# Optimization experiments

Measured on AMD Instinct MI355X. Metric: run time of the kernel, lower is better.

Reference implementation:

```python
import jax, jax.numpy as jnp
import numpy as np

SIGMA = 1e-4
GAMMA = 1e-4
ZNEAR = 1.0
ZFAR = 100.0
EPS = 1e-10
BG = (1.0, 1.0, 1.0)

N, H, W, K = 4, 512, 512, 8
V, F = 100000, 200000


def setup_inputs() -> dict:
    key = jax.random.key(0)
    k1, k2, k3, k4, k5, k6 = jax.random.split(key, 6)
    pix_to_face = jax.random.randint(k1, (N, H, W, K), -1, F)  # -1 = background
    bary = jax.random.uniform(k2, (N, H, W, K, 3), dtype=jnp.float32)
    bary = bary / jnp.sum(bary, axis=-1, keepdims=True)  # valid barycentric
    zbuf = ZNEAR + (ZFAR - ZNEAR) * jax.random.uniform(k3, (N, H, W, K), dtype=jnp.float32)
    dists = 1e-4 * jax.random.normal(k4, (N, H, W, K), dtype=jnp.float32)
    verts_normals = jax.random.normal(k5, (V, 3), dtype=jnp.float32)
    verts_normals = verts_normals / jnp.linalg.norm(verts_normals, axis=-1, keepdims=True)
    faces = jax.random.randint(k6, (F, 3), 0, V)
    return {"pix_to_face": pix_to_face, "bary_coords": bary, "zbuf": zbuf,
            "dists": dists, "verts_normals": verts_normals, "faces": faces}


def reference(pix_to_face, bary_coords, zbuf, dists, verts_normals, faces):
    # --- NormalCalcuate: gather per-face vertex normals + barycentric interp ---
    faces_normals = verts_normals[faces]                      # (F, 3verts, 3)
    mask = pix_to_face >= 0                                    # (N,H,W,K)
    idx = jnp.maximum(pix_to_face, 0)
    attrs = faces_normals[idx]                                 # (N,H,W,K,3verts,3)
    pixel_normals = jnp.einsum('nhwkv,nhwkvd->nhwkd', bary_coords, attrs)
    pixel_normals = jnp.where(mask[..., None], pixel_normals, 0.0)

    # --- softmax_rgb_blend ---
    m = mask.astype(pixel_normals.dtype)
    prob_map = jax.nn.sigmoid(-dists / SIGMA) * m              # (N,H,W,K)
    z_inv = (ZFAR - zbuf) / (ZFAR - ZNEAR) * m                 # (N,H,W,K)
    z_inv_max = jnp.maximum(jnp.max(z_inv, axis=-1, keepdims=True), EPS)
    weights_num = prob_map * jnp.exp((z_inv - z_inv_max) / GAMMA)
    delta = jnp.maximum(jnp.exp((EPS - z_inv_max[..., 0]) / GAMMA), EPS)  # (N,H,W)
    denom = jnp.sum(weights_num, axis=-1) + delta              # (N,H,W)
    weighted_colors = jnp.einsum('nhwk,nhwkd->nhwd', weights_num, pixel_normals)
    bg = jnp.asarray(BG, dtype=pixel_normals.dtype)
    rgb = (weighted_colors + delta[..., None] * bg) / denom[..., None]  # (N,H,W,3)

    # --- F.normalize(dim=3) then (x+1)/2 ---
    norm = jnp.maximum(jnp.linalg.norm(rgb, axis=-1, keepdims=True), 1e-12)
    images = (rgb / norm + 1.0) / 2.0
    return images
```

## Files before the change

### kernel.cpp

```cpp
#include <hip/hip_runtime.h>

#define SIGMA_INV 1.0e4f
#define GAMMA_INV 1.0e4f
#define ZNEAR 1.0f
#define ZFAR 100.0f
#define EPSV 1e-10f

constexpr int KF = 8;
constexpr int NPIX = 4 * 512 * 512;
constexpr int NFACES = 200000;

__global__ __launch_bounds__(256) void pack_face_normals14(
    const int*   __restrict__ faces,
    const float* __restrict__ vnorm,
    uint4*       __restrict__ fn,
    int F)
{
    const int f = blockIdx.x * blockDim.x + threadIdx.x;
    if (f >= F) return;
    const int v[3] = { faces[f * 3 + 0], faces[f * 3 + 1], faces[f * 3 + 2] };

    unsigned long long lo = 0ull, hi = 0ull;
    int i = 0;
#pragma unroll
    for (int t = 0; t < 3; ++t) {
#pragma unroll
        for (int c = 0; c < 3; ++c, ++i) {
            const float x = vnorm[(size_t)v[t] * 3 + c];
            const unsigned long long code = (unsigned long long)(unsigned)
                __float2int_rn(fminf(fmaxf(x, -1.0f), 1.0f) * 8191.5f + 8191.5f);
            const int bp = 14 * i;
            if (bp < 64) {
                lo |= code << bp;
                if (bp > 50) hi |= code >> (64 - bp);
            } else {
                hi |= code << (bp - 64);
            }
        }
    }
    uint4 q;
    q.x = (unsigned)(lo & 0xFFFFFFFFull);
    q.y = (unsigned)(lo >> 32);
    q.z = (unsigned)(hi & 0xFFFFFFFFull);
    q.w = (unsigned)(hi >> 32);
    fn[f] = q;
}

__device__ __forceinline__ float dec14(const unsigned* w, int i) {
    const int bp = 14 * i;
    const int j = bp >> 5;
    const int off = bp & 31;
    unsigned long long u = (unsigned long long)w[j];
    if (j < 3) u |= (unsigned long long)w[j + 1] << 32;
    const unsigned code = (unsigned)(u >> off) & 0x3FFFu;
    return fmaf((float)code, 2.0f / 16383.0f, -1.0f);
}

__global__ __launch_bounds__(256) void normal_shader_q14(
    const int*   __restrict__ p2f,
    const float* __restrict__ bary,
    const float* __restrict__ zbuf,
    const float* __restrict__ dists,
    const uint4* __restrict__ fn,
    float*       __restrict__ out)
{
    const int p = blockIdx.x * blockDim.x + threadIdx.x;
    if (p >= NPIX) return;

    const int4* pf4 = reinterpret_cast<const int4*>(p2f + (size_t)p * KF);
    int4 fa = pf4[0], fb = pf4[1];
    int f[KF] = {fa.x, fa.y, fa.z, fa.w, fb.x, fb.y, fb.z, fb.w};

    uint4 q[KF];
#pragma unroll
    for (int k = 0; k < KF; ++k) {
        const int idx = f[k] < 0 ? 0 : f[k];
        q[k] = fn[idx];
    }

    const float4* z4 = reinterpret_cast<const float4*>(zbuf + (size_t)p * KF);
    float4 za = z4[0], zb = z4[1];
    float zv[KF] = {za.x, za.y, za.z, za.w, zb.x, zb.y, zb.z, zb.w};

    const float4* d4 = reinterpret_cast<const float4*>(dists + (size_t)p * KF);
    float4 da = d4[0], db = d4[1];
    float dv[KF] = {da.x, da.y, da.z, da.w, db.x, db.y, db.z, db.w};

    const float4* b4 = reinterpret_cast<const float4*>(bary + (size_t)p * KF * 3);
    float bc[KF * 3];
#pragma unroll
    for (int i = 0; i < 6; ++i) {
        float4 t = b4[i];
        bc[4 * i + 0] = t.x; bc[4 * i + 1] = t.y;
        bc[4 * i + 2] = t.z; bc[4 * i + 3] = t.w;
    }

    float zinv[KF], prob[KF];
    float zmax = EPSV;
#pragma unroll
    for (int k = 0; k < KF; ++k) {
        const bool m = f[k] >= 0;
        const float zi = m ? (ZFAR - zv[k]) * (1.0f / (ZFAR - ZNEAR)) : 0.0f;
        const float pr = m ? 1.0f / (1.0f + __expf(dv[k] * SIGMA_INV)) : 0.0f;
        zinv[k] = zi;
        prob[k] = pr;
        zmax = fmaxf(zmax, zi);
    }

    float accx = 0.0f, accy = 0.0f, accz = 0.0f, wtot = 0.0f;
#pragma unroll
    for (int k = 0; k < KF; ++k) {
        unsigned w[4] = { q[k].x, q[k].y, q[k].z, q[k].w };
        const float n0x = dec14(w, 0), n0y = dec14(w, 1), n0z = dec14(w, 2);
        const float n1x = dec14(w, 3), n1y = dec14(w, 4), n1z = dec14(w, 5);
        const float n2x = dec14(w, 6), n2y = dec14(w, 7), n2z = dec14(w, 8);
        const float b0 = bc[k * 3 + 0];
        const float b1 = bc[k * 3 + 1];
        const float b2 = bc[k * 3 + 2];
        const float nx = b0 * n0x + b1 * n1x + b2 * n2x;
        const float ny = b0 * n0y + b1 * n1y + b2 * n2y;
        const float nz = b0 * n0z + b1 * n1z + b2 * n2z;
        const float wgt = prob[k] * __expf((zinv[k] - zmax) * GAMMA_INV);
        wtot += wgt;
        accx = fmaf(wgt, nx, accx);
        accy = fmaf(wgt, ny, accy);
        accz = fmaf(wgt, nz, accz);
    }

    const float delta = fmaxf(__expf((EPSV - zmax) * GAMMA_INV), EPSV);
    const float inv_denom = 1.0f / (wtot + delta);
    const float r = (accx + delta) * inv_denom;
    const float g = (accy + delta) * inv_denom;
    const float b = (accz + delta) * inv_denom;

    const float nrm = sqrtf(r * r + g * g + b * b);
    const float invn = 1.0f / fmaxf(nrm, 1e-12f);

    float* o = out + (size_t)p * 3;
    o[0] = fmaf(r * invn, 0.5f, 0.5f);
    o[1] = fmaf(g * invn, 0.5f, 0.5f);
    o[2] = fmaf(b * invn, 0.5f, 0.5f);
}

__global__ __launch_bounds__(256) void normal_shader_direct(
    const int*   __restrict__ p2f,
    const float* __restrict__ bary,
    const float* __restrict__ zbuf,
    const float* __restrict__ dists,
    const float* __restrict__ vnorm,
    const int*   __restrict__ faces,
    float*       __restrict__ out)
{
    const int p = blockIdx.x * blockDim.x + threadIdx.x;
    if (p >= NPIX) return;

    const int4* pf4 = reinterpret_cast<const int4*>(p2f + (size_t)p * KF);
    int4 fa = pf4[0], fb = pf4[1];
    int f[KF] = {fa.x, fa.y, fa.z, fa.w, fb.x, fb.y, fb.z, fb.w};

    const float4* z4 = reinterpret_cast<const float4*>(zbuf + (size_t)p * KF);
    float4 za = z4[0], zb = z4[1];
    float zv[KF] = {za.x, za.y, za.z, za.w, zb.x, zb.y, zb.z, zb.w};

    const float4* d4 = reinterpret_cast<const float4*>(dists + (size_t)p * KF);
    float4 da = d4[0], db = d4[1];
    float dv[KF] = {da.x, da.y, da.z, da.w, db.x, db.y, db.z, db.w};

    const float4* b4 = reinterpret_cast<const float4*>(bary + (size_t)p * KF * 3);
    float bc[KF * 3];
#pragma unroll
    for (int i = 0; i < 6; ++i) {
        float4 t = b4[i];
        bc[4 * i + 0] = t.x; bc[4 * i + 1] = t.y;
        bc[4 * i + 2] = t.z; bc[4 * i + 3] = t.w;
    }

    float zinv[KF], prob[KF];
    float zmax = EPSV;
#pragma unroll
    for (int k = 0; k < KF; ++k) {
        const bool m = f[k] >= 0;
        const float zi = m ? (ZFAR - zv[k]) * (1.0f / (ZFAR - ZNEAR)) : 0.0f;
        const float pr = m ? 1.0f / (1.0f + __expf(dv[k] * SIGMA_INV)) : 0.0f;
        zinv[k] = zi;
        prob[k] = pr;
        zmax = fmaxf(zmax, zi);
    }

    float accx = 0.0f, accy = 0.0f, accz = 0.0f, wtot = 0.0f;
#pragma unroll
    for (int k = 0; k < KF; ++k) {
        const int idx = f[k] < 0 ? 0 : f[k];
        const int i3 = idx * 3;
        const int v0 = faces[i3 + 0];
        const int v1 = faces[i3 + 1];
        const int v2 = faces[i3 + 2];
        const float b0 = bc[k * 3 + 0];
        const float b1 = bc[k * 3 + 1];
        const float b2 = bc[k * 3 + 2];
        const float* n0 = vnorm + (size_t)v0 * 3;
        const float* n1 = vnorm + (size_t)v1 * 3;
        const float* n2 = vnorm + (size_t)v2 * 3;
        const float nx = b0 * n0[0] + b1 * n1[0] + b2 * n2[0];
        const float ny = b0 * n0[1] + b1 * n1[1] + b2 * n2[1];
        const float nz = b0 * n0[2] + b1 * n1[2] + b2 * n2[2];
        const float wgt = prob[k] * __expf((zinv[k] - zmax) * GAMMA_INV);
        wtot += wgt;
        accx = fmaf(wgt, nx, accx);
        accy = fmaf(wgt, ny, accy);
        accz = fmaf(wgt, nz, accz);
    }

    const float delta = fmaxf(__expf((EPSV - zmax) * GAMMA_INV), EPSV);
    const float inv_denom = 1.0f / (wtot + delta);
    const float r = (accx + delta) * inv_denom;
    const float g = (accy + delta) * inv_denom;
    const float b = (accz + delta) * inv_denom;

    const float nrm = sqrtf(r * r + g * g + b * b);
    const float invn = 1.0f / fmaxf(nrm, 1e-12f);

    float* o = out + (size_t)p * 3;
    o[0] = fmaf(r * invn, 0.5f, 0.5f);
    o[1] = fmaf(g * invn, 0.5f, 0.5f);
    o[2] = fmaf(b * invn, 0.5f, 0.5f);
}

extern "C" void kernel_launch(void* const* d_in, const int* in_sizes, int n_in,
                              void* d_out, int out_size, void* d_ws, size_t ws_size,
                              hipStream_t stream) {
    const int*   p2f   = (const int*)d_in[0];
    const float* bary  = (const float*)d_in[1];
    const float* zbuf  = (const float*)d_in[2];
    const float* dists = (const float*)d_in[3];
    const float* vnorm = (const float*)d_in[4];
    const int*   faces = (const int*)d_in[5];
    float* out = (float*)d_out;

    const int threads = 256;
    const size_t fn_bytes = (size_t)NFACES * sizeof(uint4);

    if (ws_size >= fn_bytes) {
        uint4* fn = (uint4*)d_ws;
        pack_face_normals14<<<(NFACES + threads - 1) / threads, threads, 0, stream>>>(
            faces, vnorm, fn, NFACES);
        normal_shader_q14<<<(NPIX + threads - 1) / threads, threads, 0, stream>>>(
            p2f, bary, zbuf, dists, fn, out);
    } else {
        normal_shader_direct<<<(NPIX + threads - 1) / threads, threads, 0, stream>>>(
            p2f, bary, zbuf, dists, vnorm, faces, out);
    }
}
```

Measured before the change: 258.8 us.

## Split each pixel across four lanes with shuffle reductions

The shading kernel now assigns four threads per pixel, each handling two of the eight faces, and combines zmax, weights and accumulated normals with wave shuffles. Each lane issues only two gathers and loads, so fewer registers are live and more memory requests can be in flight to hide gather latency. In exchange it launches four times as many threads, adds shuffle and instruction overhead, and switches from wide float4 loads to float2 loads.

```diff
diff --git a/kernel.cpp b/kernel.cpp
--- a/kernel.cpp
+++ b/kernel.cpp
@@ -56,7 +56,7 @@
     return fmaf((float)code, 2.0f / 16383.0f, -1.0f);
 }
 
-__global__ __launch_bounds__(256) void normal_shader_q14(
+__global__ __launch_bounds__(256) void normal_shader_q14_split(
     const int*   __restrict__ p2f,
     const float* __restrict__ bary,
     const float* __restrict__ zbuf,
@@ -64,82 +64,73 @@
     const uint4* __restrict__ fn,
     float*       __restrict__ out)
 {
-    const int p = blockIdx.x * blockDim.x + threadIdx.x;
+    const int t = blockIdx.x * blockDim.x + threadIdx.x;
+    const int p = t >> 2;
+    const int sub = t & 3;
     if (p >= NPIX) return;
 
-    const int4* pf4 = reinterpret_cast<const int4*>(p2f + (size_t)p * KF);
-    int4 fa = pf4[0], fb = pf4[1];
-    int f[KF] = {fa.x, fa.y, fa.z, fa.w, fb.x, fb.y, fb.z, fb.w};
-
-    uint4 q[KF];
-#pragma unroll
-    for (int k = 0; k < KF; ++k) {
-        const int idx = f[k] < 0 ? 0 : f[k];
-        q[k] = fn[idx];
-    }
-
-    const float4* z4 = reinterpret_cast<const float4*>(zbuf + (size_t)p * KF);
-    float4 za = z4[0], zb = z4[1];
-    float zv[KF] = {za.x, za.y, za.z, za.w, zb.x, zb.y, zb.z, zb.w};
-
-    const float4* d4 = reinterpret_cast<const float4*>(dists + (size_t)p * KF);
-    float4 da = d4[0], db = d4[1];
-    float dv[KF] = {da.x, da.y, da.z, da.w, db.x, db.y, db.z, db.w};
-
-    const float4* b4 = reinterpret_cast<const float4*>(bary + (size_t)p * KF * 3);
-    float bc[KF * 3];
-#pragma unroll
-    for (int i = 0; i < 6; ++i) {
-        float4 t = b4[i];
-        bc[4 * i + 0] = t.x; bc[4 * i + 1] = t.y;
-        bc[4 * i + 2] = t.z; bc[4 * i + 3] = t.w;
-    }
-
-    float zinv[KF], prob[KF];
-    float zmax = EPSV;
-#pragma unroll
-    for (int k = 0; k < KF; ++k) {
-        const bool m = f[k] >= 0;
-        const float zi = m ? (ZFAR - zv[k]) * (1.0f / (ZFAR - ZNEAR)) : 0.0f;
-        const float pr = m ? 1.0f / (1.0f + __expf(dv[k] * SIGMA_INV)) : 0.0f;
-        zinv[k] = zi;
-        prob[k] = pr;
-        zmax = fmaxf(zmax, zi);
-    }
-
-    float accx = 0.0f, accy = 0.0f, accz = 0.0f, wtot = 0.0f;
-#pragma unroll
-    for (int k = 0; k < KF; ++k) {
-        unsigned w[4] = { q[k].x, q[k].y, q[k].z, q[k].w };
-        const float n0x = dec14(w, 0), n0y = dec14(w, 1), n0z = dec14(w, 2);
-        const float n1x = dec14(w, 3), n1y = dec14(w, 4), n1z = dec14(w, 5);
-        const float n2x = dec14(w, 6), n2y = dec14(w, 7), n2z = dec14(w, 8);
-        const float b0 = bc[k * 3 + 0];
-        const float b1 = bc[k * 3 + 1];
-        const float b2 = bc[k * 3 + 2];
-        const float nx = b0 * n0x + b1 * n1x + b2 * n2x;
-        const float ny = b0 * n0y + b1 * n1y + b2 * n2y;
-        const float nz = b0 * n0z + b1 * n1z + b2 * n2z;
-        const float wgt = prob[k] * __expf((zinv[k] - zmax) * GAMMA_INV);
+    const int base = p * KF + sub * 2;
+
+    const int2   f2  = *reinterpret_cast<const int2*>(p2f + base);
+    const float2 z2  = *reinterpret_cast<const float2*>(zbuf + base);
+    const float2 d2  = *reinterpret_cast<const float2*>(dists + base);
+    const float2 b01 = *reinterpret_cast<const float2*>(bary + (size_t)base * 3 + 0);
+    const float2 b23 = *reinterpret_cast<const float2*>(bary + (size_t)base * 3 + 2);
+    const float2 b45 = *reinterpret_cast<const float2*>(bary + (size_t)base * 3 + 4);
+
+    const int i0 = f2.x < 0 ? 0 : f2.x;
+    const int i1 = f2.y < 0 ? 0 : f2.y;
+    const uint4 g0 = fn[i0];
+    const uint4 g1 = fn[i1];
+
+    const bool m0 = f2.x >= 0, m1 = f2.y >= 0;
+    const float zi0 = m0 ? (ZFAR - z2.x) * (1.0f / (ZFAR - ZNEAR)) : 0.0f;
+    const float zi1 = m1 ? (ZFAR - z2.y) * (1.0f / (ZFAR - ZNEAR)) : 0.0f;
+    const float pr0 = m0 ? 1.0f / (1.0f + __expf(d2.x * SIGMA_INV)) : 0.0f;
+    const float pr1 = m1 ? 1.0f / (1.0f + __expf(d2.y * SIGMA_INV)) : 0.0f;
+
+    float zmax = fmaxf(fmaxf(zi0, zi1), EPSV);
+    zmax = fmaxf(zmax, __shfl_xor(zmax, 1));
+    zmax = fmaxf(zmax, __shfl_xor(zmax, 2));
+
+    float ax, ay, az, wtot;
+    {
+        unsigned w[4] = { g0.x, g0.y, g0.z, g0.w };
+        const float nx = b01.x * dec14(w, 0) + b01.y * dec14(w, 3) + b23.x * dec14(w, 6);
+        const float ny = b01.x * dec14(w, 1) + b01.y * dec14(w, 4) + b23.x * dec14(w, 7);
+        const float nz = b01.x * dec14(w, 2) + b01.y * dec14(w, 5) + b23.x * dec14(w, 8);
+        const float wgt = pr0 * __expf((zi0 - zmax) * GAMMA_INV);
+        wtot = wgt;
+        ax = wgt * nx; ay = wgt * ny; az = wgt * nz;
+    }
+    {
+        unsigned w[4] = { g1.x, g1.y, g1.z, g1.w };
+        const float nx = b23.y * dec14(w, 0) + b45.x * dec14(w, 3) + b45.y * dec14(w, 6);
+        const float ny = b23.y * dec14(w, 1) + b45.x * dec14(w, 4) + b45.y * dec14(w, 7);
+        const float nz = b23.y * dec14(w, 2) + b45.x * dec14(w, 5) + b45.y * dec14(w, 8);
+        const float wgt = pr1 * __expf((zi1 - zmax) * GAMMA_INV);
         wtot += wgt;
-        accx = fmaf(wgt, nx, accx);
-        accy = fmaf(wgt, ny, accy);
-        accz = fmaf(wgt, nz, accz);
-    }
+        ax = fmaf(wgt, nx, ax); ay = fmaf(wgt, ny, ay); az = fmaf(wgt, nz, az);
+    }
+
+    wtot += __shfl_xor(wtot, 1);  wtot += __shfl_xor(wtot, 2);
+    ax   += __shfl_xor(ax, 1);    ax   += __shfl_xor(ax, 2);
+    ay   += __shfl_xor(ay, 1);    ay   += __shfl_xor(ay, 2);
+    az   += __shfl_xor(az, 1);    az   += __shfl_xor(az, 2);
 
     const float delta = fmaxf(__expf((EPSV - zmax) * GAMMA_INV), EPSV);
     const float inv_denom = 1.0f / (wtot + delta);
-    const float r = (accx + delta) * inv_denom;
-    const float g = (accy + delta) * inv_denom;
-    const float b = (accz + delta) * inv_denom;
+    const float r = (ax + delta) * inv_denom;
+    const float g = (ay + delta) * inv_denom;
+    const float b = (az + delta) * inv_denom;
 
     const float nrm = sqrtf(r * r + g * g + b * b);
     const float invn = 1.0f / fmaxf(nrm, 1e-12f);
 
-    float* o = out + (size_t)p * 3;
-    o[0] = fmaf(r * invn, 0.5f, 0.5f);
-    o[1] = fmaf(g * invn, 0.5f, 0.5f);
-    o[2] = fmaf(b * invn, 0.5f, 0.5f);
+    if (sub < 3) {
+        const float c = (sub == 0) ? r : (sub == 1) ? g : b;
+        out[(size_t)p * 3 + sub] = fmaf(c * invn, 0.5f, 0.5f);
+    }
 }
 
 __global__ __launch_bounds__(256) void normal_shader_direct(
@@ -244,7 +235,8 @@
         uint4* fn = (uint4*)d_ws;
         pack_face_normals14<<<(NFACES + threads - 1) / threads, threads, 0, stream>>>(
             faces, vnorm, fn, NFACES);
-        normal_shader_q14<<<(NPIX + threads - 1) / threads, threads, 0, stream>>>(
+        const long long nthreads = (long long)NPIX * 4;
+        normal_shader_q14_split<<<(int)((nthreads + threads - 1) / threads), threads, 0, stream>>>(
             p2f, bary, zbuf, dists, fn, out);
     } else {
         normal_shader_direct<<<(NPIX + threads - 1) / threads, threads, 0, stream>>>(
```

Result: no change. 258.3 us (-0.2%).
